# Performance work log

Measured on AMD Instinct MI355X. Metric: run time of the kernel, lower is better.

## Reference

```python
import jax, jax.numpy as jnp
import numpy as np

B, S, D = 4, 2048, 1024
H, DK, DV, DOUT = 16, 64, 64, 1024
NEG = -1.0e9


def setup_inputs() -> dict:
    key = jax.random.key(0)
    ks = jax.random.split(key, 12)
    sq = lambda fan_in: 1.0 / np.sqrt(fan_in)
    return {
        "query": jax.random.normal(ks[0], (B, S, D), jnp.float32),
        "key": jax.random.normal(ks[1], (B, S, D), jnp.float32),
        "value": jax.random.normal(ks[2], (B, S, D), jnp.float32),
        "attention_mask": jax.random.randint(ks[3], (B, 1, 1, S), 0, 2, jnp.int32),
        "wq": jax.random.normal(ks[4], (D, H * DK), jnp.float32) * sq(D),
        "bq": jnp.zeros((H * DK,), jnp.float32),
        "wk": jax.random.normal(ks[5], (D, H * DK), jnp.float32) * sq(D),
        "bk": jnp.zeros((H * DK,), jnp.float32),
        "wv": jax.random.normal(ks[6], (D, H * DV), jnp.float32) * sq(D),
        "bv": jnp.zeros((H * DV,), jnp.float32),
        "wo": jax.random.normal(ks[7], (H * DV, DOUT), jnp.float32) * sq(H * DV),
        "bo": jnp.zeros((DOUT,), jnp.float32),
    }


def _split_heads(x, head_dim):
    b, s, _ = x.shape
    return x.reshape(b, s, H, head_dim).transpose(0, 2, 1, 3)  # [B,H,S,hd]


def reference(query, key, value, attention_mask, wq, bq, wk, bk, wv, bv, wo, bo):
    q = _split_heads(query @ wq + bq, DK)   # [B,H,S,DK]
    k = _split_heads(key @ wk + bk, DK)     # [B,H,S,DK]
    v = _split_heads(value @ wv + bv, DV)   # [B,H,S,DV]
    logits = jnp.einsum("bhqd,bhkd->bhqk", q, k) / jnp.sqrt(jnp.float32(DK))
    logits = logits + attention_mask.astype(logits.dtype) * NEG
    attn = jax.nn.softmax(logits, axis=-1)
    out = jnp.einsum("bhqk,bhkd->bhqd", attn, v)          # [B,H,S,DV]
    out = out.transpose(0, 2, 1, 3).reshape(query.shape[0], -1, H * DV)
    return out @ wo + bo
```

## Files before the change

kernel.cpp:

```cpp
#include <hip/hip_runtime.h>
#include <hip/hip_bf16.h>
#include <math.h>

#define Bv 4
#define Sv 2048
#define Dv 1024
#define Hv 16
#define HD 64
#define NEGV (-1.0e9f)

typedef __attribute__((ext_vector_type(8))) short bf16x8;
typedef __attribute__((ext_vector_type(4))) short s16x4;
typedef __attribute__((ext_vector_type(4))) float f32x4;

__device__ __forceinline__ short f2bf(float f) {
    union { __hip_bfloat16 h; short s; } u;
    u.h = __float2bfloat16(f);
    return u.s;
}

__device__ __forceinline__ void glds16(const void* g, void* l) {
    __builtin_amdgcn_global_load_lds(
        (const __attribute__((address_space(1))) void*)g,
        (__attribute__((address_space(3))) void*)l, 16, 0, 0);
}

__global__ __launch_bounds__(256) void cvt_bf16(const float* __restrict__ X,
                                                unsigned short* __restrict__ Y) {
    const size_t i = ((size_t)blockIdx.x * 256 + threadIdx.x) * 8;
    const float4 a = *(const float4*)&X[i];
    const float4 b = *(const float4*)&X[i + 4];
    bf16x8 o = {f2bf(a.x), f2bf(a.y), f2bf(a.z), f2bf(a.w),
                f2bf(b.x), f2bf(b.y), f2bf(b.z), f2bf(b.w)};
    *(bf16x8*)&Y[i] = o;
}

__global__ __launch_bounds__(256) void transpose_w(const float* __restrict__ W,
                                                   unsigned short* __restrict__ WT) {
    __shared__ float T[64][65];
    const int t = threadIdx.x;
    const int n0 = blockIdx.x * 64, k0 = blockIdx.y * 64;
    #pragma unroll
    for (int i = 0; i < 4; ++i) {
        const int k = (t >> 4) + 16 * i;
        const int nc = (t & 15) * 4;
        const float4 v = *(const float4*)&W[(size_t)(k0 + k) * 1024 + n0 + nc];
        T[k][nc + 0] = v.x; T[k][nc + 1] = v.y;
        T[k][nc + 2] = v.z; T[k][nc + 3] = v.w;
    }
    __syncthreads();
    const int n = t >> 2, kc = (t & 3) * 16;
    #pragma unroll
    for (int j4 = 0; j4 < 4; ++j4) {
        s16x4 o;
        #pragma unroll
        for (int jj = 0; jj < 4; ++jj) o[jj] = f2bf(T[kc + j4 * 4 + jj][n]);
        *(s16x4*)&WT[(size_t)(n0 + n) * 1024 + k0 + kc + j4 * 4] = o;
    }
}

__global__ __launch_bounds__(256) void transpose_v(const unsigned short* __restrict__ Vin,
                                                   unsigned short* __restrict__ VT) {
    __shared__ unsigned short T[64][72];
    const int t = threadIdx.x;
    const int s0 = blockIdx.x * 64;
    const int bh = blockIdx.y;
    const size_t ib = (size_t)bh * Sv * 64;
    const size_t ob = (size_t)bh * 64 * Sv;
    {
        const int s = t >> 2, dc = (t & 3) * 16;
        const bf16x8 a = *(const bf16x8*)&Vin[ib + (size_t)(s0 + s) * 64 + dc];
        const bf16x8 b = *(const bf16x8*)&Vin[ib + (size_t)(s0 + s) * 64 + dc + 8];
        *(bf16x8*)&T[s][dc] = a;
        *(bf16x8*)&T[s][dc + 8] = b;
    }
    __syncthreads();
    const int dv = t >> 2, sc = (t & 3) * 16;
    #pragma unroll
    for (int j4 = 0; j4 < 4; ++j4) {
        s16x4 o;
        #pragma unroll
        for (int jj = 0; jj < 4; ++jj) o[jj] = (short)T[sc + j4 * 4 + jj][dv];
        *(s16x4*)&VT[ob + (size_t)dv * Sv + s0 + sc + j4 * 4] = o;
    }
}

template <int PERM>
__global__ __launch_bounds__(256) void gemm_mfma(const unsigned short* __restrict__ X,
                                                 const unsigned short* __restrict__ WT,
                                                 const float* __restrict__ bias,
                                                 void* __restrict__ Cv,
                                                 int M, int N, int K) {
    __shared__ short As[128 * 32];
    __shared__ short Bs[128 * 32];

    const int t = threadIdx.x;
    const int lane = t & 63, w = t >> 6;
    const int l15 = lane & 15, quad = lane >> 4;
    const int m0 = blockIdx.y * 128, n0 = blockIdx.x * 128;
    const int wm = (w >> 1) * 64, wn = (w & 1) * 64;

    f32x4 acc[4][4];
    #pragma unroll
    for (int mi = 0; mi < 4; ++mi)
        #pragma unroll
        for (int ni = 0; ni < 4; ++ni) acc[mi][ni] = (f32x4){0.f, 0.f, 0.f, 0.f};

    const int srow = lane >> 2;
    const int skc = (lane & 3) * 8;

    for (int k0 = 0; k0 < K; k0 += 32) {
        #pragma unroll
        for (int i = 0; i < 2; ++i) {
            const int seg = w * 2 + i;
            const int row = seg * 16 + srow;
            glds16(&WT[(size_t)(n0 + row) * K + k0 + skc], &Bs[seg * 512]);
            glds16(&X[(size_t)(m0 + row) * K + k0 + skc], &As[seg * 512]);
        }
        __syncthreads();

        bf16x8 afr[4], bfr[4];
        #pragma unroll
        for (int mi = 0; mi < 4; ++mi)
            afr[mi] = *(const bf16x8*)&As[(wm + mi * 16 + l15) * 32 + quad * 8];
        #pragma unroll
        for (int ni = 0; ni < 4; ++ni)
            bfr[ni] = *(const bf16x8*)&Bs[(wn + ni * 16 + l15) * 32 + quad * 8];
        #pragma unroll
        for (int mi = 0; mi < 4; ++mi)
            #pragma unroll
            for (int ni = 0; ni < 4; ++ni)
                acc[mi][ni] = __builtin_amdgcn_mfma_f32_16x16x32_bf16(
                    afr[mi], bfr[ni], acc[mi][ni], 0, 0, 0);
        __syncthreads();
    }

    #pragma unroll
    for (int mi = 0; mi < 4; ++mi) {
        #pragma unroll
        for (int ni = 0; ni < 4; ++ni) {
            const int col = n0 + wn + ni * 16 + l15;
            const float bsv = bias[col];
            #pragma unroll
            for (int r = 0; r < 4; ++r) {
                const int row = m0 + wm + mi * 16 + quad * 4 + r;
                const float vv = acc[mi][ni][r] + bsv;
                if constexpr (PERM == 0) {
                    ((float*)Cv)[(size_t)row * N + col] = vv;
                } else {
                    const int bb = row / Sv, s = row % Sv;
                    const int hh = col >> 6, d = col & 63;
                    ((unsigned short*)Cv)[((((size_t)bb * Hv + hh) * Sv + s) << 6) + d] =
                        (unsigned short)f2bf(vv);
                }
            }
        }
    }
}

__global__ __launch_bounds__(256) void attn_mfma(const unsigned short* __restrict__ Q,
                                                 const unsigned short* __restrict__ Kg,
                                                 const unsigned short* __restrict__ VT,
                                                 const int* __restrict__ mask,
                                                 unsigned short* __restrict__ O) {
    __shared__ short Kl[64 * 72];
    __shared__ short Vl[64 * 72];
    __shared__ short Sl[128 * 72];
    __shared__ float Mk[64];

    const int t = threadIdx.x;
    const int lane = t & 63, w = t >> 6;
    const int l15 = lane & 15, quad = lane >> 4;
    const int q0 = blockIdx.x * 128;
    const int h = blockIdx.y, b = blockIdx.z;
    const int bh = b * Hv + h;
    const size_t kvb = (size_t)bh * Sv * 64;
    const size_t vtb = (size_t)bh * 64 * Sv;

    bf16x8 qf[2][2];
    #pragma unroll
    for (int ni = 0; ni < 2; ++ni) {
        const size_t qa = kvb + (size_t)(q0 + w * 32 + ni * 16 + l15) * 64 + quad * 8;
        qf[ni][0] = *(const bf16x8*)&Q[qa];
        qf[ni][1] = *(const bf16x8*)&Q[qa + 32];
    }

    float l_acc[2] = {0.f, 0.f};
    f32x4 oacc[2][4];
    #pragma unroll
    for (int mi = 0; mi < 2; ++mi)
        #pragma unroll
        for (int ni = 0; ni < 4; ++ni) oacc[mi][ni] = (f32x4){0.f, 0.f, 0.f, 0.f};

    const int srow = t >> 2, sch = (t & 3) * 16;

    for (int k0 = 0; k0 < Sv; k0 += 64) {
        __syncthreads();
        {
            const unsigned short* Ks = Kg + kvb + (size_t)k0 * 64;
            const bf16x8 a = *(const bf16x8*)&Ks[(size_t)srow * 64 + sch];
            const bf16x8 c = *(const bf16x8*)&Ks[(size_t)srow * 64 + sch + 8];
            *(bf16x8*)&Kl[srow * 72 + sch] = a;
            *(bf16x8*)&Kl[srow * 72 + sch + 8] = c;
            const unsigned short* Vs = VT + vtb + k0;
            const bf16x8 d = *(const bf16x8*)&Vs[(size_t)srow * Sv + sch];
            const bf16x8 e = *(const bf16x8*)&Vs[(size_t)srow * Sv + sch + 8];
            *(bf16x8*)&Vl[srow * 72 + sch] = d;
            *(bf16x8*)&Vl[srow * 72 + sch + 8] = e;
        }
        if (t < 64) Mk[t] = NEGV * (float)mask[(size_t)b * Sv + k0 + t];
        __syncthreads();

        #pragma unroll
        for (int mi = 0; mi < 4; ++mi) {
            const bf16x8 kf0 = *(const bf16x8*)&Kl[(mi * 16 + l15) * 72 + quad * 8];
            const bf16x8 kf1 = *(const bf16x8*)&Kl[(mi * 16 + l15) * 72 + 32 + quad * 8];
            const float4 mk4 = *(const float4*)&Mk[mi * 16 + quad * 4];
            #pragma unroll
            for (int ni = 0; ni < 2; ++ni) {
                f32x4 st = (f32x4){0.f, 0.f, 0.f, 0.f};
                st = __builtin_amdgcn_mfma_f32_16x16x32_bf16(kf0, qf[ni][0], st, 0, 0, 0);
                st = __builtin_amdgcn_mfma_f32_16x16x32_bf16(kf1, qf[ni][1], st, 0, 0, 0);
                const float p0 = __expf(st[0] * 0.125f + mk4.x);
                const float p1 = __expf(st[1] * 0.125f + mk4.y);
                const float p2 = __expf(st[2] * 0.125f + mk4.z);
                const float p3 = __expf(st[3] * 0.125f + mk4.w);
                l_acc[ni] += (p0 + p1) + (p2 + p3);
                s16x4 pv = {f2bf(p0), f2bf(p1), f2bf(p2), f2bf(p3)};
                *(s16x4*)&Sl[(w * 32 + ni * 16 + l15) * 72 + mi * 16 + quad * 4] = pv;
            }
        }

        #pragma unroll
        for (int mi = 0; mi < 2; ++mi) {
            const bf16x8 pf0 = *(const bf16x8*)&Sl[(w * 32 + mi * 16 + l15) * 72 + quad * 8];
            const bf16x8 pf1 = *(const bf16x8*)&Sl[(w * 32 + mi * 16 + l15) * 72 + 32 + quad * 8];
            #pragma unroll
            for (int ni = 0; ni < 4; ++ni) {
                const bf16x8 vf0 = *(const bf16x8*)&Vl[(ni * 16 + l15) * 72 + quad * 8];
                const bf16x8 vf1 = *(const bf16x8*)&Vl[(ni * 16 + l15) * 72 + 32 + quad * 8];
                oacc[mi][ni] = __builtin_amdgcn_mfma_f32_16x16x32_bf16(pf0, vf0, oacc[mi][ni], 0, 0, 0);
                oacc[mi][ni] = __builtin_amdgcn_mfma_f32_16x16x32_bf16(pf1, vf1, oacc[mi][ni], 0, 0, 0);
            }
        }
    }

    #pragma unroll
    for (int mi = 0; mi < 2; ++mi) {
        float l = l_acc[mi];
        l += __shfl_xor(l, 16);
        l += __shfl_xor(l, 32);
        #pragma unroll
        for (int r = 0; r < 4; ++r) {
            const float lr = __shfl(l, quad * 4 + r, 64);
            const float inv = 1.0f / lr;
            const size_t row = (size_t)b * Sv + q0 + w * 32 + mi * 16 + quad * 4 + r;
            #pragma unroll
            for (int ni = 0; ni < 4; ++ni) {
                O[row * (Hv * HD) + h * HD + ni * 16 + l15] =
                    (unsigned short)f2bf(oacc[mi][ni][r] * inv);
            }
        }
    }
}

extern "C" void kernel_launch(void* const* d_in, const int* in_sizes, int n_in,
                              void* d_out, int out_size, void* d_ws, size_t ws_size,
                              hipStream_t stream) {
    const float* query = (const float*)d_in[0];
    const float* key   = (const float*)d_in[1];
    const float* value = (const float*)d_in[2];
    const int*   amask = (const int*)d_in[3];
    const float* wq = (const float*)d_in[4];
    const float* bq = (const float*)d_in[5];
    const float* wk = (const float*)d_in[6];
    const float* bk = (const float*)d_in[7];
    const float* wv = (const float*)d_in[8];
    const float* bv = (const float*)d_in[9];
    const float* wo = (const float*)d_in[10];
    const float* bo = (const float*)d_in[11];
    float* out = (float*)d_out;

    unsigned short* wsp = (unsigned short*)d_ws;
    dim3 bb(256), gt(16, 16);

    if (ws_size >= (size_t)64 * 1024 * 1024) {
        const size_t PBQ = (size_t)Bv * Hv * Sv * HD;
        unsigned short* qb = wsp;
        unsigned short* kb = qb + PBQ;
        unsigned short* vb = kb + PBQ;
        unsigned short* ab = vb + PBQ;
        unsigned short* wt_kb = kb;
        unsigned short* wt_out = (unsigned short*)d_out;
        unsigned short* wt_vb = vb;

        const int M = Bv * Sv;
        dim3 gg(8, M / 128), gc(M * 1024 / 2048);

        cvt_bf16<<<gc, bb, 0, stream>>>(value, ab);
        transpose_w<<<gt, bb, 0, stream>>>(wv, wt_kb);
        gemm_mfma<1><<<gg, bb, 0, stream>>>(ab, wt_kb, bv, qb, M, 1024, 1024);
        transpose_v<<<dim3(Sv / 64, Bv * Hv), bb, 0, stream>>>(qb, vb);

        cvt_bf16<<<gc, bb, 0, stream>>>(query, ab);
        transpose_w<<<gt, bb, 0, stream>>>(wq, wt_kb);
        gemm_mfma<1><<<gg, bb, 0, stream>>>(ab, wt_kb, bq, qb, M, 1024, 1024);

        cvt_bf16<<<gc, bb, 0, stream>>>(key, ab);
        transpose_w<<<gt, bb, 0, stream>>>(wk, wt_out);
        gemm_mfma<1><<<gg, bb, 0, stream>>>(ab, wt_out, bk, kb, M, 1024, 1024);

        attn_mfma<<<dim3(Sv / 128, Hv, Bv), bb, 0, stream>>>(qb, kb, vb, amask, ab);

        transpose_w<<<gt, bb, 0, stream>>>(wo, wt_vb);
        gemm_mfma<0><<<gg, bb, 0, stream>>>(ab, wt_vb, bo, out, M, 1024, 1024);
    } else {
        const size_t PQ = (size_t)Hv * Sv * HD;
        unsigned short* qb = wsp;
        unsigned short* kb = qb + PQ;
        unsigned short* vb = kb + PQ;
        unsigned short* ab = vb + PQ;
        const int M = Sv;
        dim3 gg(8, M / 128), gc(M * 1024 / 2048);
        for (int b = 0; b < Bv; ++b) {
            const size_t xoff = (size_t)b * Sv * Dv;
            unsigned short* wt_kb = kb;
            unsigned short* wt_out = (unsigned short*)(out + xoff);
            unsigned short* wt_vb = vb;

            cvt_bf16<<<gc, bb, 0, stream>>>(value + xoff, ab);
            transpose_w<<<gt, bb, 0, stream>>>(wv, wt_kb);
            gemm_mfma<1><<<gg, bb, 0, stream>>>(ab, wt_kb, bv, qb, M, 1024, 1024);
            transpose_v<<<dim3(Sv / 64, Hv), bb, 0, stream>>>(qb, vb);

            cvt_bf16<<<gc, bb, 0, stream>>>(query + xoff, ab);
            transpose_w<<<gt, bb, 0, stream>>>(wq, wt_kb);
            gemm_mfma<1><<<gg, bb, 0, stream>>>(ab, wt_kb, bq, qb, M, 1024, 1024);

            cvt_bf16<<<gc, bb, 0, stream>>>(key + xoff, ab);
            transpose_w<<<gt, bb, 0, stream>>>(wk, wt_out);
            gemm_mfma<1><<<gg, bb, 0, stream>>>(ab, wt_out, bk, kb, M, 1024, 1024);

            attn_mfma<<<dim3(Sv / 128, Hv, 1), bb, 0, stream>>>(qb, kb, vb,
                                                                amask + (size_t)b * Sv, ab);

            transpose_w<<<gt, bb, 0, stream>>>(wo, wt_vb);
            gemm_mfma<0><<<gg, bb, 0, stream>>>(ab, wt_vb, bo, out + xoff, M, 1024, 1024);
        }
    }
}
```

Baseline: 409.3 us.

## Batch Q/K projections, fuse V transpose into GEMM epilogue, fold softmax scale into Wq

The Q and K conversions, weight transposes and GEMMs now run as single launches, with the z grid dimension picking the operand. The V projection GEMM writes its output already transposed, which removes the separate transpose_v kernel. The softmax scale and log2(e) factor are folded into Wq and bq so attention can use exp2f without a multiply. Other changes: a cheaper f2bf rounding, a padded score tile stride in LDS, and a flattened attention grid that puts heads and batches in the fast-varying index. The new f2bf rounding differs slightly from the library conversion for NaN and rounding ties.

```diff
diff --git a/kernel.cpp b/kernel.cpp
--- a/kernel.cpp
+++ b/kernel.cpp
@@ -8,15 +8,14 @@
 #define Hv 16
 #define HD 64
 #define NEGV (-1.0e9f)
+#define QSCALE 0.1803368867f
 
 typedef __attribute__((ext_vector_type(8))) short bf16x8;
 typedef __attribute__((ext_vector_type(4))) short s16x4;
 typedef __attribute__((ext_vector_type(4))) float f32x4;
 
 __device__ __forceinline__ short f2bf(float f) {
-    union { __hip_bfloat16 h; short s; } u;
-    u.h = __float2bfloat16(f);
-    return u.s;
+    return (short)((__float_as_uint(f) + 0x8000u) >> 16);
 }
 
 __device__ __forceinline__ void glds16(const void* g, void* l) {
@@ -25,8 +24,12 @@
         (__attribute__((address_space(3))) void*)l, 16, 0, 0);
 }
 
-__global__ __launch_bounds__(256) void cvt_bf16(const float* __restrict__ X,
-                                                unsigned short* __restrict__ Y) {
+__global__ __launch_bounds__(256) void cvt2(const float* __restrict__ X0,
+                                            unsigned short* __restrict__ Y0,
+                                            const float* __restrict__ X1,
+                                            unsigned short* __restrict__ Y1) {
+    const float* X = blockIdx.y ? X1 : X0;
+    unsigned short* Y = blockIdx.y ? Y1 : Y0;
     const size_t i = ((size_t)blockIdx.x * 256 + threadIdx.x) * 8;
     const float4 a = *(const float4*)&X[i];
     const float4 b = *(const float4*)&X[i + 4];
@@ -35,8 +38,15 @@
     *(bf16x8*)&Y[i] = o;
 }
 
-__global__ __launch_bounds__(256) void transpose_w(const float* __restrict__ W,
-                                                   unsigned short* __restrict__ WT) {
+__global__ __launch_bounds__(256) void transpose_w2(const float* __restrict__ W0,
+                                                    unsigned short* __restrict__ T0o,
+                                                    float s0,
+                                                    const float* __restrict__ W1,
+                                                    unsigned short* __restrict__ T1o,
+                                                    float s1) {
+    const float* W = blockIdx.z ? W1 : W0;
+    unsigned short* WT = blockIdx.z ? T1o : T0o;
+    const float sc = blockIdx.z ? s1 : s0;
     __shared__ float T[64][65];
     const int t = threadIdx.x;
     const int n0 = blockIdx.x * 64, k0 = blockIdx.y * 64;
@@ -54,43 +64,17 @@
     for (int j4 = 0; j4 < 4; ++j4) {
         s16x4 o;
         #pragma unroll
-        for (int jj = 0; jj < 4; ++jj) o[jj] = f2bf(T[kc + j4 * 4 + jj][n]);
+        for (int jj = 0; jj < 4; ++jj) o[jj] = f2bf(T[kc + j4 * 4 + jj][n] * sc);
         *(s16x4*)&WT[(size_t)(n0 + n) * 1024 + k0 + kc + j4 * 4] = o;
     }
 }
 
-__global__ __launch_bounds__(256) void transpose_v(const unsigned short* __restrict__ Vin,
-                                                   unsigned short* __restrict__ VT) {
-    __shared__ unsigned short T[64][72];
-    const int t = threadIdx.x;
-    const int s0 = blockIdx.x * 64;
-    const int bh = blockIdx.y;
-    const size_t ib = (size_t)bh * Sv * 64;
-    const size_t ob = (size_t)bh * 64 * Sv;
-    {
-        const int s = t >> 2, dc = (t & 3) * 16;
-        const bf16x8 a = *(const bf16x8*)&Vin[ib + (size_t)(s0 + s) * 64 + dc];
-        const bf16x8 b = *(const bf16x8*)&Vin[ib + (size_t)(s0 + s) * 64 + dc + 8];
-        *(bf16x8*)&T[s][dc] = a;
-        *(bf16x8*)&T[s][dc + 8] = b;
-    }
-    __syncthreads();
-    const int dv = t >> 2, sc = (t & 3) * 16;
-    #pragma unroll
-    for (int j4 = 0; j4 < 4; ++j4) {
-        s16x4 o;
-        #pragma unroll
-        for (int jj = 0; jj < 4; ++jj) o[jj] = (short)T[sc + j4 * 4 + jj][dv];
-        *(s16x4*)&VT[ob + (size_t)dv * Sv + s0 + sc + j4 * 4] = o;
-    }
-}
-
 template <int PERM>
-__global__ __launch_bounds__(256) void gemm_mfma(const unsigned short* __restrict__ X,
-                                                 const unsigned short* __restrict__ WT,
-                                                 const float* __restrict__ bias,
-                                                 void* __restrict__ Cv,
-                                                 int M, int N, int K) {
+__device__ __forceinline__ void gemm_core(const unsigned short* __restrict__ X,
+                                          const unsigned short* __restrict__ WT,
+                                          const float* __restrict__ bias,
+                                          float bscale, void* __restrict__ Cv,
+                                          int M, int N, int K) {
     __shared__ short As[128 * 32];
     __shared__ short Bs[128 * 32];
 
@@ -140,42 +124,82 @@
         #pragma unroll
         for (int ni = 0; ni < 4; ++ni) {
             const int col = n0 + wn + ni * 16 + l15;
-            const float bsv = bias[col];
-            #pragma unroll
-            for (int r = 0; r < 4; ++r) {
-                const int row = m0 + wm + mi * 16 + quad * 4 + r;
-                const float vv = acc[mi][ni][r] + bsv;
-                if constexpr (PERM == 0) {
-                    ((float*)Cv)[(size_t)row * N + col] = vv;
-                } else {
-                    const int bb = row / Sv, s = row % Sv;
-                    const int hh = col >> 6, d = col & 63;
-                    ((unsigned short*)Cv)[((((size_t)bb * Hv + hh) * Sv + s) << 6) + d] =
-                        (unsigned short)f2bf(vv);
+            const float bsv = bias[col] * bscale;
+            if constexpr (PERM == 2) {
+                const int r0 = m0 + wm + mi * 16 + quad * 4;
+                const int bb = r0 / Sv, s = r0 % Sv;
+                const int hh = col >> 6, d = col & 63;
+                s16x4 ov = {f2bf(acc[mi][ni][0] + bsv), f2bf(acc[mi][ni][1] + bsv),
+                            f2bf(acc[mi][ni][2] + bsv), f2bf(acc[mi][ni][3] + bsv)};
+                *(s16x4*)&((unsigned short*)Cv)[(((size_t)bb * Hv + hh) * 64 + d) * Sv + s] = ov;
+            } else {
+                #pragma unroll
+                for (int r = 0; r < 4; ++r) {
+                    const int row = m0 + wm + mi * 16 + quad * 4 + r;
+                    const float vv = acc[mi][ni][r] + bsv;
+                    if constexpr (PERM == 0) {
+                        ((float*)Cv)[(size_t)row * N + col] = vv;
+                    } else {
+                        const int bb = row / Sv, s = row % Sv;
+                        const int hh = col >> 6, d = col & 63;
+                        ((unsigned short*)Cv)[((((size_t)bb * Hv + hh) * Sv + s) << 6) + d] =
+                            (unsigned short)f2bf(vv);
+                    }
                 }
             }
         }
     }
+}
+
+__global__ __launch_bounds__(256) void gemm_qk(const unsigned short* Xq,
+                                               const unsigned short* WTq,
+                                               const float* bq, float sq,
+                                               unsigned short* Cq,
+                                               const unsigned short* Xk,
+                                               const unsigned short* WTk,
+                                               const float* bk,
+                                               unsigned short* Ck,
+                                               int M, int N, int K) {
+    const bool z = blockIdx.z != 0;
+    gemm_core<1>(z ? Xk : Xq, z ? WTk : WTq, z ? bk : bq, z ? 1.0f : sq,
+                 z ? Ck : Cq, M, N, K);
+}
+
+__global__ __launch_bounds__(256) void gemm_v(const unsigned short* X,
+                                              const unsigned short* WT,
+                                              const float* bias,
+                                              unsigned short* C,
+                                              int M, int N, int K) {
+    gemm_core<2>(X, WT, bias, 1.0f, C, M, N, K);
+}
+
+__global__ __launch_bounds__(256) void gemm_o(const unsigned short* X,
+                                              const unsigned short* WT,
+                                              const float* bias, float* C,
+                                              int M, int N, int K) {
+    gemm_core<0>(X, WT, bias, 1.0f, C, M, N, K);
 }
 
 __global__ __launch_bounds__(256) void attn_mfma(const unsigned short* __restrict__ Q,
                                                  const unsigned short* __restrict__ Kg,
                                                  const unsigned short* __restrict__ VT,
                                                  const int* __restrict__ mask,
-                                                 unsigned short* __restrict__ O) {
+                                                 unsigned short* __restrict__ O,
+                                                 int nbh) {
     __shared__ short Kl[64 * 72];
     __shared__ short Vl[64 * 72];
-    __shared__ short Sl[128 * 72];
+    __shared__ short Sl[128 * 76];
     __shared__ float Mk[64];
 
     const int t = threadIdx.x;
     const int lane = t & 63, w = t >> 6;
     const int l15 = lane & 15, quad = lane >> 4;
-    const int q0 = blockIdx.x * 128;
-    const int h = blockIdx.y, b = blockIdx.z;
-    const int bh = b * Hv + h;
-    const size_t kvb = (size_t)bh * Sv * 64;
-    const size_t vtb = (size_t)bh * 64 * Sv;
+    const int bidx = blockIdx.x;
+    const int hb = bidx % nbh;
+    const int q0 = (bidx / nbh) * 128;
+    const int b = hb >> 4, h = hb & 15;
+    const size_t kvb = (size_t)hb * Sv * 64;
+    const size_t vtb = (size_t)hb * 64 * Sv;
 
     bf16x8 qf[2][2];
     #pragma unroll
@@ -221,20 +245,20 @@
                 f32x4 st = (f32x4){0.f, 0.f, 0.f, 0.f};
                 st = __builtin_amdgcn_mfma_f32_16x16x32_bf16(kf0, qf[ni][0], st, 0, 0, 0);
                 st = __builtin_amdgcn_mfma_f32_16x16x32_bf16(kf1, qf[ni][1], st, 0, 0, 0);
-                const float p0 = __expf(st[0] * 0.125f + mk4.x);
-                const float p1 = __expf(st[1] * 0.125f + mk4.y);
-                const float p2 = __expf(st[2] * 0.125f + mk4.z);
-                const float p3 = __expf(st[3] * 0.125f + mk4.w);
+                const float p0 = exp2f(st[0] + mk4.x);
+                const float p1 = exp2f(st[1] + mk4.y);
+                const float p2 = exp2f(st[2] + mk4.z);
+                const float p3 = exp2f(st[3] + mk4.w);
                 l_acc[ni] += (p0 + p1) + (p2 + p3);
                 s16x4 pv = {f2bf(p0), f2bf(p1), f2bf(p2), f2bf(p3)};
-                *(s16x4*)&Sl[(w * 32 + ni * 16 + l15) * 72 + mi * 16 + quad * 4] = pv;
+                *(s16x4*)&Sl[(w * 32 + ni * 16 + l15) * 76 + mi * 16 + quad * 4] = pv;
             }
         }
 
         #pragma unroll
         for (int mi = 0; mi < 2; ++mi) {
-            const bf16x8 pf0 = *(const bf16x8*)&Sl[(w * 32 + mi * 16 + l15) * 72 + quad * 8];
-            const bf16x8 pf1 = *(const bf16x8*)&Sl[(w * 32 + mi * 16 + l15) * 72 + 32 + quad * 8];
+            const bf16x8 pf0 = *(const bf16x8*)&Sl[(w * 32 + mi * 16 + l15) * 76 + quad * 8];
+            const bf16x8 pf1 = *(const bf16x8*)&Sl[(w * 32 + mi * 16 + l15) * 76 + 32 + quad * 8];
             #pragma unroll
             for (int ni = 0; ni < 4; ++ni) {
                 const bf16x8 vf0 = *(const bf16x8*)&Vl[(ni * 16 + l15) * 72 + quad * 8];
@@ -282,7 +306,7 @@
     float* out = (float*)d_out;
 
     unsigned short* wsp = (unsigned short*)d_ws;
-    dim3 bb(256), gt(16, 16);
+    dim3 bb(256);
 
     if (ws_size >= (size_t)64 * 1024 * 1024) {
         const size_t PBQ = (size_t)Bv * Hv * Sv * HD;
@@ -290,30 +314,27 @@
         unsigned short* kb = qb + PBQ;
         unsigned short* vb = kb + PBQ;
         unsigned short* ab = vb + PBQ;
-        unsigned short* wt_kb = kb;
-        unsigned short* wt_out = (unsigned short*)d_out;
-        unsigned short* wt_vb = vb;
+        unsigned short* xk = (unsigned short*)d_out;
+        unsigned short* wtq = vb;
+        unsigned short* wtk = vb + 1024 * 1024;
+        unsigned short* wtv = (unsigned short*)d_out;
+        unsigned short* wto = qb;
 
         const int M = Bv * Sv;
-        dim3 gg(8, M / 128), gc(M * 1024 / 2048);
-
-        cvt_bf16<<<gc, bb, 0, stream>>>(value, ab);
-        transpose_w<<<gt, bb, 0, stream>>>(wv, wt_kb);
-        gemm_mfma<1><<<gg, bb, 0, stream>>>(ab, wt_kb, bv, qb, M, 1024, 1024);
-        transpose_v<<<dim3(Sv / 64, Bv * Hv), bb, 0, stream>>>(qb, vb);
-
-        cvt_bf16<<<gc, bb, 0, stream>>>(query, ab);
-        transpose_w<<<gt, bb, 0, stream>>>(wq, wt_kb);
-        gemm_mfma<1><<<gg, bb, 0, stream>>>(ab, wt_kb, bq, qb, M, 1024, 1024);
-
-        cvt_bf16<<<gc, bb, 0, stream>>>(key, ab);
-        transpose_w<<<gt, bb, 0, stream>>>(wk, wt_out);
-        gemm_mfma<1><<<gg, bb, 0, stream>>>(ab, wt_out, bk, kb, M, 1024, 1024);
-
-        attn_mfma<<<dim3(Sv / 128, Hv, Bv), bb, 0, stream>>>(qb, kb, vb, amask, ab);
-
-        transpose_w<<<gt, bb, 0, stream>>>(wo, wt_vb);
-        gemm_mfma<0><<<gg, bb, 0, stream>>>(ab, wt_vb, bo, out, M, 1024, 1024);
+
+        cvt2<<<dim3(4096, 2), bb, 0, stream>>>(query, ab, key, xk);
+        transpose_w2<<<dim3(16, 16, 2), bb, 0, stream>>>(wq, wtq, QSCALE, wk, wtk, 1.0f);
+        gemm_qk<<<dim3(8, 64, 2), bb, 0, stream>>>(ab, wtq, bq, QSCALE, qb,
+                                                   xk, wtk, bk, kb, M, 1024, 1024);
+
+        cvt2<<<dim3(4096, 1), bb, 0, stream>>>(value, ab, value, ab);
+        transpose_w2<<<dim3(16, 16, 1), bb, 0, stream>>>(wv, wtv, 1.0f, wv, wtv, 1.0f);
+        gemm_v<<<dim3(8, 64), bb, 0, stream>>>(ab, wtv, bv, vb, M, 1024, 1024);
+
+        attn_mfma<<<dim3(16 * 64), bb, 0, stream>>>(qb, kb, vb, amask, ab, 64);
+
+        transpose_w2<<<dim3(16, 16, 1), bb, 0, stream>>>(wo, wto, 1.0f, wo, wto, 1.0f);
+        gemm_o<<<dim3(8, 64), bb, 0, stream>>>(ab, wto, bo, out, M, 1024, 1024);
     } else {
         const size_t PQ = (size_t)Hv * Sv * HD;
         unsigned short* qb = wsp;
@@ -321,31 +342,28 @@
         unsigned short* vb = kb + PQ;
         unsigned short* ab = vb + PQ;
         const int M = Sv;
-        dim3 gg(8, M / 128), gc(M * 1024 / 2048);
         for (int b = 0; b < Bv; ++b) {
             const size_t xoff = (size_t)b * Sv * Dv;
-            unsigned short* wt_kb = kb;
-            unsigned short* wt_out = (unsigned short*)(out + xoff);
-            unsigned short* wt_vb = vb;
-
-            cvt_bf16<<<gc, bb, 0, stream>>>(value + xoff, ab);
-            transpose_w<<<gt, bb, 0, stream>>>(wv, wt_kb);
-            gemm_mfma<1><<<gg, bb, 0, stream>>>(ab, wt_kb, bv, qb, M, 1024, 1024);
-            transpose_v<<<dim3(Sv / 64, Hv), bb, 0, stream>>>(qb, vb);
-
-            cvt_bf16<<<gc, bb, 0, stream>>>(query + xoff, ab);
-            transpose_w<<<gt, bb, 0, stream>>>(wq, wt_kb);
-            gemm_mfma<1><<<gg, bb, 0, stream>>>(ab, wt_kb, bq, qb, M, 1024, 1024);
-
-            cvt_bf16<<<gc, bb, 0, stream>>>(key + xoff, ab);
-            transpose_w<<<gt, bb, 0, stream>>>(wk, wt_out);
-            gemm_mfma<1><<<gg, bb, 0, stream>>>(ab, wt_out, bk, kb, M, 1024, 1024);
-
-            attn_mfma<<<dim3(Sv / 128, Hv, 1), bb, 0, stream>>>(qb, kb, vb,
-                                                                amask + (size_t)b * Sv, ab);
-
-            transpose_w<<<gt, bb, 0, stream>>>(wo, wt_vb);
-            gemm_mfma<0><<<gg, bb, 0, stream>>>(ab, wt_vb, bo, out + xoff, M, 1024, 1024);
-        }
-    }
-}
+            unsigned short* xk = (unsigned short*)(out + xoff);
+            unsigned short* wtq = vb;
+            unsigned short* wtk = vb + 1024 * 1024;
+            unsigned short* wtv = xk;
+            unsigned short* wto = qb;
+
+            cvt2<<<dim3(1024, 2), bb, 0, stream>>>(query + xoff, ab, key + xoff, xk);
+            transpose_w2<<<dim3(16, 16, 2), bb, 0, stream>>>(wq, wtq, QSCALE, wk, wtk, 1.0f);
+            gemm_qk<<<dim3(8, 16, 2), bb, 0, stream>>>(ab, wtq, bq, QSCALE, qb,
+                                                       xk, wtk, bk, kb, M, 1024, 1024);
+
+            cvt2<<<dim3(1024, 1), bb, 0, stream>>>(value + xoff, ab, value + xoff, ab);
+            transpose_w2<<<dim3(16, 16, 1), bb, 0, stream>>>(wv, wtv, 1.0f, wv, wtv, 1.0f);
+            gemm_v<<<dim3(8, 16), bb, 0, stream>>>(ab, wtv, bv, vb, M, 1024, 1024);
+
+            attn_mfma<<<dim3(16 * 16), bb, 0, stream>>>(qb, kb, vb, amask + (size_t)b * Sv,
+                                                        ab, 16);
+
+            transpose_w2<<<dim3(16, 16, 1), bb, 0, stream>>>(wo, wto, 1.0f, wo, wto, 1.0f);
+            gemm_o<<<dim3(8, 16), bb, 0, stream>>>(ab, wto, bo, out + xoff, M, 1024, 1024);
+        }
+    }
+}
```

Measured after the change: 411.4 us. About the same (+0.5%).
